# Performance work log

Hardware: AMD Instinct MI355X
Metric: run time of the kernel (lower is better)

The kernel has to match this reference:

```python
import jax, jax.numpy as jnp
import numpy as np

D_MODEL = 1024
N_HEADS = 16
MAX_SEQ = 1024
BATCH = 4

def _first_primes(n):
    limit = n * 15
    sieve = np.ones(limit, dtype=bool)
    sieve[:2] = False
    for i in range(2, int(limit ** 0.5) + 1):
        if sieve[i]:
            sieve[i * i::i] = False
    return np.flatnonzero(sieve)[:n]

def _pi_attention_bias(n_heads, max_seq_len):
    # bias[h, t, s] = 0.1 * sin(prime[h]*pi * (t - s) / max_seq_len)
    primes = _first_primes(n_heads).astype(np.float32)
    freqs = primes * np.pi  # [H]
    pos = np.arange(max_seq_len, dtype=np.float32)
    pos_diff = pos[:, None] - pos[None, :]  # [T, T]
    bias = np.sin(freqs[:, None, None] * pos_diff[None] / max_seq_len) * 0.1
    return jnp.asarray(bias, dtype=jnp.float32)

def setup_inputs() -> dict:
    key = jax.random.key(0)
    ks = jax.random.split(key, 8)
    D = D_MODEL
    xavier = (6.0 / (D + D)) ** 0.5
    inp = {
        'x': jax.random.normal(ks[0], (BATCH, MAX_SEQ, D), dtype=jnp.float32),
        'Wq': jax.random.uniform(ks[1], (D, D), jnp.float32, -xavier, xavier),
        'bq': jnp.zeros((D,), jnp.float32),
        'Wk': jax.random.uniform(ks[2], (D, D), jnp.float32, -xavier, xavier),
        'bk': jnp.zeros((D,), jnp.float32),
        'Wv': jax.random.uniform(ks[3], (D, D), jnp.float32, -xavier, xavier),
        'bv': jnp.zeros((D,), jnp.float32),
        'Wo': jax.random.uniform(ks[4], (D, D), jnp.float32, -xavier, xavier),
        'bo': jnp.zeros((D,), jnp.float32),
        'pi_bias': _pi_attention_bias(N_HEADS, MAX_SEQ),
        'bias_scale': jnp.asarray(0.1, jnp.float32),
        'spectral_alpha': jnp.asarray(1.0, jnp.float32),
    }
    return inp

def reference(x, Wq, bq, Wk, bk, Wv, bv, Wo, bo, pi_bias, bias_scale, spectral_alpha):
    B, T, D = x.shape
    H = N_HEADS
    hd = D // H
    scale = 1.0 / (hd ** 0.5)

    def split_heads(y):
        return y.reshape(B, T, H, hd).transpose(0, 2, 1, 3)  # [B,H,T,hd]

    q = split_heads(x @ Wq + bq)
    k = split_heads(x @ Wk + bk)
    v = split_heads(x @ Wv + bv)

    # spectral filter along the time axis (use_spectral and T > 4)
    freqs = jnp.fft.fftfreq(T).astype(jnp.float32)  # [T]
    filt = jnp.exp(-jnp.abs(spectral_alpha) * jnp.abs(freqs))[None, None, :, None]
    q = jnp.fft.ifft(jnp.fft.fft(q, axis=2, norm='ortho') * filt, axis=2, norm='ortho').real
    k = jnp.fft.ifft(jnp.fft.fft(k, axis=2, norm='ortho') * filt, axis=2, norm='ortho').real

    scores = jnp.einsum('bhtd,bhsd->bhts', q, k) * scale
    scores = scores + bias_scale * pi_bias[None, :, :T, :T]
    attn = jax.nn.softmax(scores, axis=-1)  # dropout is identity in eval
    out = jnp.einsum('bhts,bhsd->bhtd', attn, v)
    out = out.transpose(0, 2, 1, 3).reshape(B, T, D)
    return out @ Wo + bo
```

## Files before the change

### kernel.cpp

```cpp
#include <hip/hip_runtime.h>
#include <hip/hip_bf16.h>

typedef __bf16 bf16x8 __attribute__((ext_vector_type(8)));
typedef float f32x4 __attribute__((ext_vector_type(4)));

#define OFF_G      0x0ULL
#define OFF_GMAT   0x10000ULL
#define OFF_XB     0x210000ULL
#define OFF_XBT    0xA10000ULL
#define OFF_XF     0x1210000ULL
#define OFF_WQT    0x1A10000ULL
#define OFF_WKT    0x1C10000ULL
#define OFF_WVT    0x1E10000ULL
#define OFF_WOT    0x2010000ULL
#define OFF_KB     0x2210000ULL
#define OFF_VTB    0x2A10000ULL

static __device__ __forceinline__ unsigned short f2bf(float f) {
  union { float f; unsigned int u; } v; v.f = f;
  unsigned int r = v.u + 0x7FFFu + ((v.u >> 16) & 1u);
  return (unsigned short)(r >> 16);
}

static __device__ __forceinline__ void g2l16(const unsigned short* g, unsigned short* l) {
  __builtin_amdgcn_global_load_lds(
      (const __attribute__((address_space(1))) unsigned int*)g,
      (__attribute__((address_space(3))) unsigned int*)l, 16, 0, 0);
}

__constant__ float PRIMES_F[16] = {2.f, 3.f, 5.f, 7.f, 11.f, 13.f, 17.f, 19.f,
                                   23.f, 29.f, 31.f, 37.f, 41.f, 43.f, 47.f, 53.f};

__global__ __launch_bounds__(256) void k_g(const float* __restrict__ alpha_p,
                                           float* __restrict__ g) {
  const int d = blockIdx.x;
  const float alpha = fabsf(alpha_p[0]);
  float partial = 0.f;
  for (int j = threadIdx.x; j < 1024; j += 256) {
    int jm = (j <= 512) ? j : 1024 - j;
    float filt = expf(-alpha * (float)jm * (1.0f / 1024.f));
    int p = (j * d) & 1023;
    partial += filt * cosf((float)p * (6.28318530717958647692f / 1024.f));
  }
  __shared__ float red[4];
  #pragma unroll
  for (int off = 32; off > 0; off >>= 1) partial += __shfl_down(partial, off, 64);
  if ((threadIdx.x & 63) == 0) red[threadIdx.x >> 6] = partial;
  __syncthreads();
  if (threadIdx.x == 0) g[d] = (red[0] + red[1] + red[2] + red[3]) * (1.f / 1024.f);
}

__global__ __launch_bounds__(256) void k_gmat(const float* __restrict__ g,
                                              unsigned short* __restrict__ Gm) {
  int i = blockIdx.x * 256 + threadIdx.x;
  int t = i >> 10, s = i & 1023;
  Gm[i] = f2bf(g[(t - s) & 1023]);
}

__global__ __launch_bounds__(256) void k_xprep(const float* __restrict__ in,
                                               unsigned short* __restrict__ xb,
                                               unsigned short* __restrict__ xbT) {
  __shared__ float tile[32][33];
  const long zoff = (long)blockIdx.z << 20;
  const int r0 = blockIdx.y * 32, c0 = blockIdx.x * 32;
  const int tx = threadIdx.x & 31, ty = threadIdx.x >> 5;
  #pragma unroll
  for (int i = 0; i < 4; i++) {
    float v = in[zoff + (long)(r0 + ty + 8 * i) * 1024 + c0 + tx];
    tile[ty + 8 * i][tx] = v;
    xb[zoff + (long)(r0 + ty + 8 * i) * 1024 + c0 + tx] = f2bf(v);
  }
  __syncthreads();
  #pragma unroll
  for (int i = 0; i < 4; i++)
    xbT[zoff + (long)(c0 + ty + 8 * i) * 1024 + r0 + tx] = f2bf(tile[tx][ty + 8 * i]);
}

__global__ __launch_bounds__(256) void k_wt(const float* __restrict__ w0,
                                            const float* __restrict__ w1,
                                            const float* __restrict__ w2,
                                            const float* __restrict__ w3,
                                            unsigned short* __restrict__ out) {
  __shared__ float tile[32][33];
  const int z = blockIdx.z;
  const float* in = (z == 0) ? w0 : (z == 1) ? w1 : (z == 2) ? w2 : w3;
  const long zoff = (long)z << 20;
  const int r0 = blockIdx.y * 32, c0 = blockIdx.x * 32;
  const int tx = threadIdx.x & 31, ty = threadIdx.x >> 5;
  #pragma unroll
  for (int i = 0; i < 4; i++)
    tile[ty + 8 * i][tx] = in[(long)(r0 + ty + 8 * i) * 1024 + c0 + tx];
  __syncthreads();
  #pragma unroll
  for (int i = 0; i < 4; i++)
    out[zoff + (long)(c0 + ty + 8 * i) * 1024 + r0 + tx] = f2bf(tile[tx][ty + 8 * i]);
}

#define GEMM_CORE(A_, Bt_, ACC_)                                                     \
  const int tid = threadIdx.x, l = tid & 63, wid = tid >> 6;                         \
  const int lr = l & 15, lg = l >> 4;                                                \
  const int wm = (wid >> 1) * 64, wn = (wid & 1) * 64;                               \
  const int srow = wid * 32 + (l >> 3);                                              \
  const int scol = ((l & 7) ^ (l >> 3)) * 8;                                         \
  const unsigned short* Ag = A_ + (long)(m0 + srow) * 1024 + scol;                   \
  const unsigned short* Bg = Bt_ + (long)(n0 + srow) * 1024 + scol;                  \
  unsigned short* Asw = As + wid * 32 * 64;                                          \
  unsigned short* Bsw = Bs + wid * 32 * 64;                                          \
  const int xk = (lr & 7) << 4;                                                      \
  const int co[2] = {(0 + lg * 16) ^ xk, (64 + lg * 16) ^ xk};                       \
  for (int kt = 0; kt < 1024; kt += 64) {                                            \
    __syncthreads();                                                                 \
    _Pragma("unroll")                                                                \
    for (int c = 0; c < 4; c++) {                                                    \
      g2l16(Ag + (long)c * 8 * 1024 + kt, Asw + c * 8 * 64);                         \
      g2l16(Bg + (long)c * 8 * 1024 + kt, Bsw + c * 8 * 64);                         \
    }                                                                                \
    __syncthreads();                                                                 \
    const char* Ab = (const char*)As;                                                \
    const char* Bb = (const char*)Bs;                                                \
    _Pragma("unroll")                                                                \
    for (int ks = 0; ks < 2; ks++) {                                                 \
      bf16x8 af[4], bfr[4];                                                          \
      _Pragma("unroll")                                                              \
      for (int mf = 0; mf < 4; mf++)                                                 \
        af[mf] = *(const bf16x8*)(Ab + (wm + mf * 16 + lr) * 128 + co[ks]);          \
      _Pragma("unroll")                                                              \
      for (int nf = 0; nf < 4; nf++)                                                 \
        bfr[nf] = *(const bf16x8*)(Bb + (wn + nf * 16 + lr) * 128 + co[ks]);         \
      _Pragma("unroll")                                                              \
      for (int mf = 0; mf < 4; mf++)                                                 \
        _Pragma("unroll")                                                            \
        for (int nf = 0; nf < 4; nf++)                                               \
          ACC_[mf][nf] = __builtin_amdgcn_mfma_f32_16x16x32_bf16(af[mf], bfr[nf],    \
                                                                 ACC_[mf][nf], 0, 0, 0); \
    }                                                                                \
  }

template <int MODE>
__global__ __launch_bounds__(256) void k_gemm(
    const unsigned short* __restrict__ A, const unsigned short* __restrict__ Bt,
    const float* __restrict__ bias, const float* __restrict__ bias2,
    void* __restrict__ Cv, void* __restrict__ Cv2, int N) {
  __shared__ __align__(16) unsigned short As[128 * 64];
  __shared__ __align__(16) unsigned short Bs[128 * 64];
  const int cpx = gridDim.x >> 3;
  const int orig = (blockIdx.x & 7) * cpx + (blockIdx.x >> 3);
  const int m0 = (orig & 31) * 128, n0 = (orig >> 5) * 128;
  f32x4 acc[4][4] = {};
  GEMM_CORE(A, Bt, acc)
  #pragma unroll
  for (int nf = 0; nf < 4; nf++) {
    const int n = n0 + wn + nf * 16 + lr;
    float bb = 0.f;
    if (MODE == 3) bb = bias[n];
    if (MODE == 5) bb = (n < 1024) ? bias[n] : bias2[n - 1024];
    #pragma unroll
    for (int mf = 0; mf < 4; mf++) {
      const int mb = m0 + wm + mf * 16 + lg * 4;
      #pragma unroll
      for (int r = 0; r < 4; r++) {
        const int m = mb + r;
        float v = acc[mf][nf][r] + bb;
        if (MODE == 3) {
          ((float*)Cv)[(long)m * N + n] = v;
        } else {
          unsigned short* Cd = (n < 1024) ? (unsigned short*)Cv : (unsigned short*)Cv2;
          Cd[(long)m * 1024 + (n & 1023)] = f2bf(v);
        }
      }
    }
  }
}

__global__ __launch_bounds__(256) void k_fv(
    const unsigned short* __restrict__ Gm, const unsigned short* __restrict__ xbT,
    const unsigned short* __restrict__ WvT, const unsigned short* __restrict__ xb,
    const float* __restrict__ bv, unsigned short* __restrict__ Xf,
    unsigned short* __restrict__ Vtb) {
  __shared__ __align__(16) unsigned short As[128 * 64];
  __shared__ __align__(16) unsigned short Bs[128 * 64];
  const int orig = (blockIdx.x & 7) * 64 + (blockIdx.x >> 3);
  const bool isV = orig >= 256;
  const int o = isV ? orig - 256 : orig;
  const int m0 = (o & 7) * 128, n0 = (o >> 3) * 128;
  const unsigned short* A_ = isV ? WvT : Gm;
  const unsigned short* Bt_ = isV ? xb : xbT;
  f32x4 acc[4][4] = {};
  GEMM_CORE(A_, Bt_, acc)
  #pragma unroll
  for (int nf = 0; nf < 4; nf++) {
    const int n = n0 + wn + nf * 16 + lr;
    #pragma unroll
    for (int mf = 0; mf < 4; mf++) {
      const int mb = wm + mf * 16 + lg * 4;
      #pragma unroll
      for (int r = 0; r < 4; r++) {
        const int m = m0 + mb + r;
        float v = acc[mf][nf][r];
        if (isV) {
          Vtb[(long)m * 4096 + n] = f2bf(v + bv[m]);
        } else {
          Xf[(long)((n & ~1023) + m) * 1024 + (n & 1023)] = f2bf(v);
        }
      }
    }
  }
}

__global__ __launch_bounds__(512) void k_attn(
    const unsigned short* __restrict__ Qb, const unsigned short* __restrict__ Kb,
    const unsigned short* __restrict__ Vtb,
    const float* __restrict__ bias_scale_p, unsigned short* __restrict__ Ob) {
  __shared__ __align__(16) unsigned short Kbuf[2][64 * 64];
  __shared__ __align__(16) unsigned short Vbuf[2][64 * 64];
  __shared__ __align__(16) unsigned short Ps[8][16 * 64];
  const int qt = blockIdx.x, h = blockIdx.y, b = blockIdx.z;
  const int tid = threadIdx.x, l = tid & 63, wid = tid >> 6;
  const int lr = l & 15, lg = l >> 4;
  const int q0 = qt * 128;
  const float LOG2E = 1.44269504088896f;
  const float c10 = bias_scale_p[0] * 0.1f * LOG2E;
  const float k1 = 0.125f * LOG2E;
  const float fh = PRIMES_F[h] * 3.14159265358979323846f;
  const unsigned short* Vth = Vtb + (long)h * 64 * 4096 + b * 1024;
  const int xk = (lr & 7) << 4;
  const int co[2] = {(0 + lg * 16) ^ xk, (64 + lg * 16) ^ xk};
  const int scol = ((l & 7) ^ (l >> 3)) * 8;

  const unsigned short* kg = Kb + (long)(b * 1024 + wid * 8 + (l >> 3)) * 1024 + h * 64 + scol;
  const unsigned short* vg = Vth + (long)(wid * 8 + (l >> 3)) * 4096 + scol;
  unsigned short* kb0 = &Kbuf[0][wid * 8 * 64];
  unsigned short* kb1 = &Kbuf[1][wid * 8 * 64];
  unsigned short* vb0 = &Vbuf[0][wid * 8 * 64];
  unsigned short* vb1 = &Vbuf[1][wid * 8 * 64];
  #define STAGE_TO(KD, VD) \
    { g2l16(kg, KD); g2l16(vg, VD); kg += 64 * 1024; vg += 64; }

  STAGE_TO(kb0, vb0);

  bf16x8 af[2];
  #pragma unroll
  for (int ks = 0; ks < 2; ks++)
    af[ks] = *(const bf16x8*)(
        &Qb[(long)(b * 1024 + q0 + wid * 16 + lr) * 1024 + h * 64 + ks * 32 + lg * 8]);

  float st2[4], ct2[4];
  #pragma unroll
  for (int r = 0; r < 4; r++) {
    float tt = (float)(q0 + wid * 16 + lg * 4 + r);
    float s_, c_;
    __sincosf(fh * tt * (1.f / 1024.f), &s_, &c_);
    st2[r] = c10 * s_;
    ct2[r] = c10 * c_;
  }
  float ss4[4], cs4[4], sd, cd;
  __sincosf(fh * (1.f / 16.f), &sd, &cd);
  #pragma unroll
  for (int nf = 0; nf < 4; nf++)
    __sincosf(fh * (float)(nf * 16 + lr) * (1.f / 1024.f), &ss4[nf], &cs4[nf]);

  f32x4 acc_o[4] = {};
  float pden[4] = {};
  __syncthreads();

  for (int it = 0; it < 16; ++it) {
    const int cur = it & 1;
    if (it < 15) {
      if (cur) { STAGE_TO(kb0, vb0); } else { STAGE_TO(kb1, vb1); }
      asm volatile("s_waitcnt vmcnt(2)" ::: "memory");
    } else {
      asm volatile("s_waitcnt vmcnt(0)" ::: "memory");
    }
    __builtin_amdgcn_s_barrier();
    __builtin_amdgcn_sched_barrier(0);
    const char* Kbb = (const char*)&Kbuf[cur][0];
    const char* Vbb = (const char*)&Vbuf[cur][0];
    f32x4 accs[4] = {};
    #pragma unroll
    for (int ks = 0; ks < 2; ks++) {
      bf16x8 bfr[4];
      #pragma unroll
      for (int nf = 0; nf < 4; nf++)
        bfr[nf] = *(const bf16x8*)(Kbb + (nf * 16 + lr) * 128 + co[ks]);
      __builtin_amdgcn_s_setprio(1);
      #pragma unroll
      for (int nf = 0; nf < 4; nf++)
        accs[nf] = __builtin_amdgcn_mfma_f32_16x16x32_bf16(af[ks], bfr[nf], accs[nf], 0, 0, 0);
      __builtin_amdgcn_s_setprio(0);
    }
    char* Pw = (char*)&Ps[wid][0];
    #pragma unroll
    for (int nf = 0; nf < 4; nf++) {
      #pragma unroll
      for (int r = 0; r < 4; r++) {
        float v = fmaf(accs[nf][r], k1, fmaf(st2[r], cs4[nf], -ct2[r] * ss4[nf]));
        float p;
        asm("v_exp_f32 %0, %1" : "=v"(p) : "v"(v));
        pden[r] += p;
        union { float f; unsigned int u; } pu; pu.f = p;
        const int prow = lg * 4 + r;
        *(unsigned short*)(Pw + prow * 128 + ((nf * 32 + lr * 2) ^ ((prow & 7) << 4))) =
            (unsigned short)((pu.u + 0x8000u) >> 16);
      }
    }
    #pragma unroll
    for (int ks = 0; ks < 2; ks++) {
      bf16x8 pa = *(const bf16x8*)(Pw + lr * 128 + co[ks]);
      bf16x8 vb[4];
      #pragma unroll
      for (int nf = 0; nf < 4; nf++)
        vb[nf] = *(const bf16x8*)(Vbb + (nf * 16 + lr) * 128 + co[ks]);
      __builtin_amdgcn_s_setprio(1);
      #pragma unroll
      for (int nf = 0; nf < 4; nf++)
        acc_o[nf] = __builtin_amdgcn_mfma_f32_16x16x32_bf16(pa, vb[nf], acc_o[nf], 0, 0, 0);
      __builtin_amdgcn_s_setprio(0);
    }
    __builtin_amdgcn_sched_barrier(0);
    __builtin_amdgcn_s_barrier();
    #pragma unroll
    for (int nf = 0; nf < 4; nf++) {
      float c_ = cs4[nf] * cd - ss4[nf] * sd;
      ss4[nf] = ss4[nf] * cd + cs4[nf] * sd;
      cs4[nf] = c_;
    }
  }
  #undef STAGE_TO
  #pragma unroll
  for (int r = 0; r < 4; r++) {
    float dsum = pden[r];
    #pragma unroll
    for (int off = 1; off < 16; off <<= 1) dsum += __shfl_xor(dsum, off, 64);
    pden[r] = 1.0f / dsum;
  }
  const int tg = q0 + wid * 16 + lg * 4;
  #pragma unroll
  for (int nf = 0; nf < 4; nf++) {
    const int dd = nf * 16 + lr;
    #pragma unroll
    for (int r = 0; r < 4; r++) {
      float val = acc_o[nf][r] * pden[r];
      Ob[(long)(b * 1024 + tg + r) * 1024 + h * 64 + dd] = f2bf(val);
    }
  }
}

extern "C" void kernel_launch(void* const* d_in, const int* in_sizes, int n_in,
                              void* d_out, int out_size, void* d_ws, size_t ws_size,
                              hipStream_t stream) {
  const float* x   = (const float*)d_in[0];
  const float* Wq  = (const float*)d_in[1];
  const float* bq  = (const float*)d_in[2];
  const float* Wk  = (const float*)d_in[3];
  const float* bk  = (const float*)d_in[4];
  const float* Wv  = (const float*)d_in[5];
  const float* bv  = (const float*)d_in[6];
  const float* Wo  = (const float*)d_in[7];
  const float* bo  = (const float*)d_in[8];
  const float* bsc = (const float*)d_in[10];
  const float* alp = (const float*)d_in[11];
  char* ws = (char*)d_ws;
  float*          g   = (float*)(ws + OFF_G);
  unsigned short* Gm  = (unsigned short*)(ws + OFF_GMAT);
  unsigned short* xb  = (unsigned short*)(ws + OFF_XB);
  unsigned short* xbT = (unsigned short*)(ws + OFF_XBT);
  unsigned short* Xf  = (unsigned short*)(ws + OFF_XF);
  unsigned short* WqT = (unsigned short*)(ws + OFF_WQT);
  unsigned short* WvT = (unsigned short*)(ws + OFF_WVT);
  unsigned short* WoT = (unsigned short*)(ws + OFF_WOT);
  unsigned short* Qb  = xbT;
  unsigned short* Kb  = (unsigned short*)(ws + OFF_KB);
  unsigned short* Vtb = (unsigned short*)(ws + OFF_VTB);
  unsigned short* Ob  = Xf;

  k_g    <<<1024, 256, 0, stream>>>(alp, g);
  k_gmat <<<4096, 256, 0, stream>>>(g, Gm);
  k_xprep<<<dim3(32, 32, 4), 256, 0, stream>>>(x, xb, xbT);
  k_wt   <<<dim3(32, 32, 4), 256, 0, stream>>>(Wq, Wk, Wv, Wo, WqT);
  k_fv<<<512, 256, 0, stream>>>(Gm, xbT, WvT, xb, bv, Xf, Vtb);
  k_gemm<5><<<512, 256, 0, stream>>>(Xf, WqT, bq, bk, Qb, Kb, 2048);
  k_attn<<<dim3(8, 16, 4), 512, 0, stream>>>(Qb, Kb, Vtb, bsc, Ob);
  k_gemm<3><<<256, 256, 0, stream>>>(Ob, WoT, bo, nullptr, d_out, nullptr, 1024);
}
```

Before: 130.8 us.

## Merge prep kernels, retile output GEMM, remap attention blocks, use fast math

Fuses the x-conversion and weight-transpose kernels into one launch to save a kernel launch. Replaces the output-projection GEMM with a 64x128-tile variant, doubling its block count to 512 for better CU occupancy. Flattens the attention grid with a block-index remap that groups heads and batches across XCDs for cache locality. Switches expf/cosf to fast intrinsics in the filter-coefficient kernel, at a small accuracy cost.

```diff
diff --git a/kernel.cpp b/kernel.cpp
--- a/kernel.cpp
+++ b/kernel.cpp
@@ -38,9 +38,9 @@
   float partial = 0.f;
   for (int j = threadIdx.x; j < 1024; j += 256) {
     int jm = (j <= 512) ? j : 1024 - j;
-    float filt = expf(-alpha * (float)jm * (1.0f / 1024.f));
+    float filt = __expf(-alpha * (float)jm * (1.0f / 1024.f));
     int p = (j * d) & 1023;
-    partial += filt * cosf((float)p * (6.28318530717958647692f / 1024.f));
+    partial += filt * __cosf((float)p * (6.28318530717958647692f / 1024.f));
   }
   __shared__ float red[4];
   #pragma unroll
@@ -57,43 +57,30 @@
   Gm[i] = f2bf(g[(t - s) & 1023]);
 }
 
-__global__ __launch_bounds__(256) void k_xprep(const float* __restrict__ in,
-                                               unsigned short* __restrict__ xb,
-                                               unsigned short* __restrict__ xbT) {
+__global__ __launch_bounds__(256) void k_prep(
+    const float* __restrict__ x, const float* __restrict__ w0,
+    const float* __restrict__ w1, const float* __restrict__ w2,
+    const float* __restrict__ w3, unsigned short* __restrict__ xb,
+    unsigned short* __restrict__ xbT, unsigned short* __restrict__ Wout) {
   __shared__ float tile[32][33];
-  const long zoff = (long)blockIdx.z << 20;
+  const int z = blockIdx.z;
+  const bool isX = z < 4;
+  const float* in = isX ? (x + ((long)z << 20))
+                        : (z == 4 ? w0 : z == 5 ? w1 : z == 6 ? w2 : w3);
+  const long ooff = isX ? ((long)z << 20) : ((long)(z - 4) << 20);
   const int r0 = blockIdx.y * 32, c0 = blockIdx.x * 32;
   const int tx = threadIdx.x & 31, ty = threadIdx.x >> 5;
   #pragma unroll
   for (int i = 0; i < 4; i++) {
-    float v = in[zoff + (long)(r0 + ty + 8 * i) * 1024 + c0 + tx];
+    float v = in[(long)(r0 + ty + 8 * i) * 1024 + c0 + tx];
     tile[ty + 8 * i][tx] = v;
-    xb[zoff + (long)(r0 + ty + 8 * i) * 1024 + c0 + tx] = f2bf(v);
+    if (isX) xb[ooff + (long)(r0 + ty + 8 * i) * 1024 + c0 + tx] = f2bf(v);
   }
   __syncthreads();
+  unsigned short* outT = isX ? xbT : Wout;
   #pragma unroll
   for (int i = 0; i < 4; i++)
-    xbT[zoff + (long)(c0 + ty + 8 * i) * 1024 + r0 + tx] = f2bf(tile[tx][ty + 8 * i]);
-}
-
-__global__ __launch_bounds__(256) void k_wt(const float* __restrict__ w0,
-                                            const float* __restrict__ w1,
-                                            const float* __restrict__ w2,
-                                            const float* __restrict__ w3,
-                                            unsigned short* __restrict__ out) {
-  __shared__ float tile[32][33];
-  const int z = blockIdx.z;
-  const float* in = (z == 0) ? w0 : (z == 1) ? w1 : (z == 2) ? w2 : w3;
-  const long zoff = (long)z << 20;
-  const int r0 = blockIdx.y * 32, c0 = blockIdx.x * 32;
-  const int tx = threadIdx.x & 31, ty = threadIdx.x >> 5;
-  #pragma unroll
-  for (int i = 0; i < 4; i++)
-    tile[ty + 8 * i][tx] = in[(long)(r0 + ty + 8 * i) * 1024 + c0 + tx];
-  __syncthreads();
-  #pragma unroll
-  for (int i = 0; i < 4; i++)
-    out[zoff + (long)(c0 + ty + 8 * i) * 1024 + r0 + tx] = f2bf(tile[tx][ty + 8 * i]);
+    outT[ooff + (long)(c0 + ty + 8 * i) * 1024 + r0 + tx] = f2bf(tile[tx][ty + 8 * i]);
 }
 
 #define GEMM_CORE(A_, Bt_, ACC_)                                                     \
@@ -136,38 +123,27 @@
     }                                                                                \
   }
 
-template <int MODE>
-__global__ __launch_bounds__(256) void k_gemm(
+__global__ __launch_bounds__(256) void k_gemm5(
     const unsigned short* __restrict__ A, const unsigned short* __restrict__ Bt,
     const float* __restrict__ bias, const float* __restrict__ bias2,
-    void* __restrict__ Cv, void* __restrict__ Cv2, int N) {
+    unsigned short* __restrict__ Cv, unsigned short* __restrict__ Cv2) {
   __shared__ __align__(16) unsigned short As[128 * 64];
   __shared__ __align__(16) unsigned short Bs[128 * 64];
-  const int cpx = gridDim.x >> 3;
-  const int orig = (blockIdx.x & 7) * cpx + (blockIdx.x >> 3);
+  const int orig = (blockIdx.x & 7) * 64 + (blockIdx.x >> 3);
   const int m0 = (orig & 31) * 128, n0 = (orig >> 5) * 128;
   f32x4 acc[4][4] = {};
   GEMM_CORE(A, Bt, acc)
   #pragma unroll
   for (int nf = 0; nf < 4; nf++) {
     const int n = n0 + wn + nf * 16 + lr;
-    float bb = 0.f;
-    if (MODE == 3) bb = bias[n];
-    if (MODE == 5) bb = (n < 1024) ? bias[n] : bias2[n - 1024];
+    const float bb = (n < 1024) ? bias[n] : bias2[n - 1024];
+    unsigned short* Cd = (n < 1024) ? Cv : Cv2;
     #pragma unroll
     for (int mf = 0; mf < 4; mf++) {
       const int mb = m0 + wm + mf * 16 + lg * 4;
       #pragma unroll
-      for (int r = 0; r < 4; r++) {
-        const int m = mb + r;
-        float v = acc[mf][nf][r] + bb;
-        if (MODE == 3) {
-          ((float*)Cv)[(long)m * N + n] = v;
-        } else {
-          unsigned short* Cd = (n < 1024) ? (unsigned short*)Cv : (unsigned short*)Cv2;
-          Cd[(long)m * 1024 + (n & 1023)] = f2bf(v);
-        }
-      }
+      for (int r = 0; r < 4; r++)
+        Cd[(long)(mb + r) * 1024 + (n & 1023)] = f2bf(acc[mf][nf][r] + bb);
     }
   }
 }
@@ -207,6 +183,65 @@
   }
 }
 
+__global__ __launch_bounds__(256) void k_gemmO(
+    const unsigned short* __restrict__ A, const unsigned short* __restrict__ Bt,
+    const float* __restrict__ bias, float* __restrict__ C) {
+  __shared__ __align__(16) unsigned short As[64 * 64];
+  __shared__ __align__(16) unsigned short Bs[128 * 64];
+  const int orig = (blockIdx.x & 7) * 64 + (blockIdx.x >> 3);
+  const int m0 = (orig & 63) * 64, n0 = (orig >> 6) * 128;
+  const int tid = threadIdx.x, l = tid & 63, wid = tid >> 6;
+  const int lr = l & 15, lg = l >> 4;
+  const int wm = (wid >> 1) * 32, wn = (wid & 1) * 64;
+  const int scol = ((l & 7) ^ (l >> 3)) * 8;
+  const unsigned short* Ag = A + (long)(m0 + wid * 16 + (l >> 3)) * 1024 + scol;
+  const unsigned short* Bg = Bt + (long)(n0 + wid * 32 + (l >> 3)) * 1024 + scol;
+  unsigned short* Asw = As + wid * 16 * 64;
+  unsigned short* Bsw = Bs + wid * 32 * 64;
+  const int xk = (lr & 7) << 4;
+  const int co[2] = {(0 + lg * 16) ^ xk, (64 + lg * 16) ^ xk};
+  f32x4 acc[2][4] = {};
+  for (int kt = 0; kt < 1024; kt += 64) {
+    __syncthreads();
+    #pragma unroll
+    for (int c = 0; c < 2; c++)
+      g2l16(Ag + (long)c * 8 * 1024 + kt, Asw + c * 8 * 64);
+    #pragma unroll
+    for (int c = 0; c < 4; c++)
+      g2l16(Bg + (long)c * 8 * 1024 + kt, Bsw + c * 8 * 64);
+    __syncthreads();
+    const char* Ab = (const char*)As;
+    const char* Bb = (const char*)Bs;
+    #pragma unroll
+    for (int ks = 0; ks < 2; ks++) {
+      bf16x8 af[2], bfr[4];
+      #pragma unroll
+      for (int mf = 0; mf < 2; mf++)
+        af[mf] = *(const bf16x8*)(Ab + (wm + mf * 16 + lr) * 128 + co[ks]);
+      #pragma unroll
+      for (int nf = 0; nf < 4; nf++)
+        bfr[nf] = *(const bf16x8*)(Bb + (wn + nf * 16 + lr) * 128 + co[ks]);
+      #pragma unroll
+      for (int mf = 0; mf < 2; mf++)
+        #pragma unroll
+        for (int nf = 0; nf < 4; nf++)
+          acc[mf][nf] = __builtin_amdgcn_mfma_f32_16x16x32_bf16(af[mf], bfr[nf], acc[mf][nf], 0, 0, 0);
+    }
+  }
+  #pragma unroll
+  for (int nf = 0; nf < 4; nf++) {
+    const int n = n0 + wn + nf * 16 + lr;
+    const float bb = bias[n];
+    #pragma unroll
+    for (int mf = 0; mf < 2; mf++) {
+      const int mb = m0 + wm + mf * 16 + lg * 4;
+      #pragma unroll
+      for (int r = 0; r < 4; r++)
+        C[(long)(mb + r) * 1024 + n] = acc[mf][nf][r] + bb;
+    }
+  }
+}
+
 __global__ __launch_bounds__(512) void k_attn(
     const unsigned short* __restrict__ Qb, const unsigned short* __restrict__ Kb,
     const unsigned short* __restrict__ Vtb,
@@ -214,7 +249,10 @@
   __shared__ __align__(16) unsigned short Kbuf[2][64 * 64];
   __shared__ __align__(16) unsigned short Vbuf[2][64 * 64];
   __shared__ __align__(16) unsigned short Ps[8][16 * 64];
-  const int qt = blockIdx.x, h = blockIdx.y, b = blockIdx.z;
+  const int bid = blockIdx.x;
+  const int qt = (bid >> 3) & 7;
+  const int hb = ((bid >> 6) << 3) | (bid & 7);
+  const int h = hb & 15, b = hb >> 4;
   const int tid = threadIdx.x, l = tid & 63, wid = tid >> 6;
   const int lr = l & 15, lg = l >> 4;
   const int q0 = qt * 128;
@@ -373,12 +411,11 @@
   unsigned short* Vtb = (unsigned short*)(ws + OFF_VTB);
   unsigned short* Ob  = Xf;
 
-  k_g    <<<1024, 256, 0, stream>>>(alp, g);
-  k_gmat <<<4096, 256, 0, stream>>>(g, Gm);
-  k_xprep<<<dim3(32, 32, 4), 256, 0, stream>>>(x, xb, xbT);
-  k_wt   <<<dim3(32, 32, 4), 256, 0, stream>>>(Wq, Wk, Wv, Wo, WqT);
+  k_g   <<<1024, 256, 0, stream>>>(alp, g);
+  k_gmat<<<4096, 256, 0, stream>>>(g, Gm);
+  k_prep<<<dim3(32, 32, 8), 256, 0, stream>>>(x, Wq, Wk, Wv, Wo, xb, xbT, WqT);
   k_fv<<<512, 256, 0, stream>>>(Gm, xbT, WvT, xb, bv, Xf, Vtb);
-  k_gemm<5><<<512, 256, 0, stream>>>(Xf, WqT, bq, bk, Qb, Kb, 2048);
-  k_attn<<<dim3(8, 16, 4), 512, 0, stream>>>(Qb, Kb, Vtb, bsc, Ob);
-  k_gemm<3><<<256, 256, 0, stream>>>(Ob, WoT, bo, nullptr, d_out, nullptr, 1024);
-}
+  k_gemm5<<<512, 256, 0, stream>>>(Xf, WqT, bq, bk, Qb, Kb);
+  k_attn<<<512, 512, 0, stream>>>(Qb, Kb, Vtb, bsc, Ob);
+  k_gemmO<<<512, 256, 0, stream>>>(Ob, WoT, bo, (float*)d_out);
+}
```

Result: faster. 123.2 us (-5.8%).
